# Kernel tuning notes

Hardware: AMD Instinct MI355X
Metric: run time of the kernel (lower is better)

Reference implementation:

```python
import jax, jax.numpy as jnp
import numpy as np

BN_EPS = 1e-5


def setup_inputs() -> dict:
    key = jax.random.key(0)
    ks = jax.random.split(key, 13)
    B, C, H, W = 8, 256, 96, 32
    D = C // 2  # inter_channels
    s = 0.05
    return {
        "x": jax.random.normal(ks[0], (B, C, H, W), jnp.float32),
        "g_w": jax.random.normal(ks[1], (D, C), jnp.float32) * s,
        "g_b": jax.random.normal(ks[2], (D,), jnp.float32) * s,
        "theta_w": jax.random.normal(ks[3], (D, C), jnp.float32) * s,
        "theta_b": jax.random.normal(ks[4], (D,), jnp.float32) * s,
        "phi_w": jax.random.normal(ks[5], (D, C), jnp.float32) * s,
        "phi_b": jax.random.normal(ks[6], (D,), jnp.float32) * s,
        "w_w": jax.random.normal(ks[7], (C, D), jnp.float32) * s,
        "w_b": jax.random.normal(ks[8], (C,), jnp.float32) * s,
        "bn_gamma": jax.random.normal(ks[9], (C,), jnp.float32),
        "bn_beta": jax.random.normal(ks[10], (C,), jnp.float32) * s,
        "bn_mean": jax.random.normal(ks[11], (C,), jnp.float32) * s,
        "bn_var": jax.random.uniform(ks[12], (C,), jnp.float32),
    }


def reference(x, g_w, g_b, theta_w, theta_b, phi_w, phi_b, w_w, w_b,
              bn_gamma, bn_beta, bn_mean, bn_var):
    B, C, H, W = x.shape
    N = H * W
    xf = x.reshape(B, C, N)  # flatten spatial: (B, C, N)

    # 1x1 conv projections == per-pixel linear maps
    g_x = jnp.einsum('dc,bcn->bnd', g_w, xf) + g_b            # (B, N, D)
    theta_x = jnp.einsum('dc,bcn->bnd', theta_w, xf) + theta_b  # (B, N, D)
    phi_x = jnp.einsum('dc,bcn->bdn', phi_w, xf) + phi_b[:, None]  # (B, D, N)

    # unnormalized attention: f = theta phi^T / N, then y = f g
    f_div_C = jnp.einsum('bnd,bdm->bnm', theta_x, phi_x) / N  # (B, N, N)
    y = jnp.einsum('bnm,bmd->bnd', f_div_C, g_x)              # (B, N, D)

    # output 1x1 conv + eval-mode BatchNorm2d
    wy = jnp.einsum('cd,bnd->bcn', w_w, y) + w_b[:, None]     # (B, C, N)
    inv = bn_gamma / jnp.sqrt(bn_var + BN_EPS)
    wy = (wy - bn_mean[:, None]) * inv[:, None] + bn_beta[:, None]

    z = wy.reshape(B, C, H, W) + x  # residual
    return z
```

## Files before the change

kernel.cpp:

```cpp
#include <hip/hip_runtime.h>
#include <hip/hip_bf16.h>
#include <cstddef>

typedef __attribute__((ext_vector_type(8))) short short8;
typedef __attribute__((ext_vector_type(4))) float floatx4;
typedef __hip_bfloat16 bf16;

#define NB 8
#define NC 256
#define ND 128
#define NN 3072
#define BN_EPS 1e-5f
#define MSPLIT 24

static __device__ __forceinline__ short f2s(float v) {
    bf16 h = __float2bfloat16(v);
    return *reinterpret_cast<short*>(&h);
}

__global__ __launch_bounds__(256) void setup_kernel(
    const float* __restrict__ phi_w, const float* __restrict__ g_w,
    const float* __restrict__ theta_w,
    const float* __restrict__ phi_b, const float* __restrict__ g_b,
    const float* __restrict__ theta_b,
    const float* __restrict__ w_b, const float* __restrict__ gamma,
    const float* __restrict__ beta, const float* __restrict__ mean,
    const float* __restrict__ var,
    short* __restrict__ Wall, float* __restrict__ bcat384,
    float* __restrict__ invv, float* __restrict__ bias2,
    float* __restrict__ Mbuf)
{
    int t = threadIdx.x;
    int r = blockIdx.x;
    if (r < 384) {
        const float* src = (r < ND) ? (phi_w + (size_t)r * NC)
                         : (r < NC) ? (g_w + (size_t)(r - ND) * NC)
                                    : (theta_w + (size_t)(r - NC) * NC);
        Wall[(size_t)r * NC + t] = f2s(src[t]);
        if (t == 0)
            bcat384[r] = (r < ND) ? phi_b[r]
                       : (r < NC) ? g_b[r - ND] : theta_b[r - NC];
        if (r == 0) {
            float iv = gamma[t] * rsqrtf(var[t] + BN_EPS);
            invv[t] = iv;
            bias2[t] = iv * (w_b[t] - mean[t]) + beta[t];
        }
    } else {
        floatx4 z = {0.f, 0.f, 0.f, 0.f};
        *(floatx4*)(Mbuf + ((size_t)(r - 384) * 256 + t) * 4) = z;
    }
}

__global__ __launch_bounds__(768)
void proj_kernel(const float* __restrict__ x, const short* __restrict__ Wall,
                 const float* __restrict__ bcat384,
                 short* __restrict__ projbuf, short* __restrict__ thND)
{
    __shared__ short Xs[128][72];
    int b = blockIdx.y;
    int n0 = blockIdx.x * 128;
    int t = threadIdx.x;
    int lane = t & 63;
    int wave = t >> 6;
    int wm = wave >> 1;
    int wn = wave & 1;
    int lm = lane & 15;
    int lk = (lane >> 4) * 8;
    int sn = t & 127;
    int scg = t >> 7;

    const float* xb = x + (size_t)b * NC * NN;

    floatx4 zero = {0.f, 0.f, 0.f, 0.f};
    floatx4 acc[4][4];
#pragma unroll
    for (int i = 0; i < 4; ++i)
#pragma unroll
        for (int j = 0; j < 4; ++j) acc[i][j] = zero;

    for (int kt = 0; kt < NC; kt += 64) {
        __syncthreads();
        if (scg < 4) {
            const float* src = xb + (size_t)(kt + scg * 16) * NN + n0 + sn;
            float v[16];
#pragma unroll
            for (int j = 0; j < 16; ++j) v[j] = src[(size_t)j * NN];
            short8 s0, s1;
#pragma unroll
            for (int j = 0; j < 8; ++j) { s0[j] = f2s(v[j]); s1[j] = f2s(v[8 + j]); }
            *(short8*)&Xs[sn][scg * 16]     = s0;
            *(short8*)&Xs[sn][scg * 16 + 8] = s1;
        }
        __syncthreads();
#pragma unroll
        for (int kk = 0; kk < 64; kk += 32) {
            short8 af[4], bfr[4];
#pragma unroll
            for (int i = 0; i < 4; ++i)
                af[i] = *(const short8*)(Wall +
                        (size_t)(wm * 64 + i * 16 + lm) * NC + kt + kk + lk);
#pragma unroll
            for (int j = 0; j < 4; ++j)
                bfr[j] = *(const short8*)&Xs[wn * 64 + j * 16 + lm][kk + lk];
#pragma unroll
            for (int i = 0; i < 4; ++i)
#pragma unroll
                for (int j = 0; j < 4; ++j)
                    acc[i][j] = __builtin_amdgcn_mfma_f32_16x16x32_bf16(
                        af[i], bfr[j], acc[i][j], 0, 0, 0);
        }
    }

    int row0 = wm * 64 + (lane >> 4) * 4;
    int col0 = n0 + wn * 64 + lm;

    if (wm < 4) {
        short* Cb = projbuf + (size_t)b * NC * NN;
#pragma unroll
        for (int i = 0; i < 4; ++i) {
#pragma unroll
            for (int r = 0; r < 4; ++r) {
                int row = row0 + i * 16 + r;
                float bv = bcat384[row];
#pragma unroll
                for (int j = 0; j < 4; ++j)
                    Cb[(size_t)row * NN + col0 + j * 16] =
                        f2s(acc[i][j][r] + bv);
            }
        }
    } else {
        short* Tb = thND + (size_t)b * NN * ND;
#pragma unroll
        for (int i = 0; i < 4; ++i) {
#pragma unroll
            for (int r = 0; r < 4; ++r) {
                int d = row0 - 256 + i * 16 + r;
                float bv = bcat384[256 + d];
#pragma unroll
                for (int j = 0; j < 4; ++j)
                    Tb[(size_t)(col0 + j * 16) * ND + d] =
                        f2s(acc[i][j][r] + bv);
            }
        }
    }
}

__global__ __launch_bounds__(256)
void bt_gemm(const short* __restrict__ Ag0, const short* __restrict__ Bg0,
             void* __restrict__ Cout, const float* __restrict__ bias,
             const float* __restrict__ resid,
             int M, int N, int K,
             long sA, long sB, long sC, long sR,
             int mode)
{
    __shared__ short As[128][72];
    __shared__ short Bs[128][72];
    int b = blockIdx.z;
    const short* Ag = Ag0 + (size_t)b * sA;
    const short* Bg = Bg0 + (size_t)b * sB;
    int tile_m = blockIdx.y * 128;
    int tile_n = blockIdx.x * 128;
    int t = threadIdx.x;
    int lane = t & 63;
    int wave = t >> 6;
    int wr = wave >> 1, wc = wave & 1;
    int lm = lane & 15;
    int lk = (lane >> 4) * 8;
    int ch = (t & 7) * 8;
    int r0 = t >> 3;

    floatx4 zero = {0.f, 0.f, 0.f, 0.f};
    floatx4 acc[4][4];
#pragma unroll
    for (int i = 0; i < 4; ++i)
#pragma unroll
        for (int j = 0; j < 4; ++j) acc[i][j] = zero;

    for (int kt = 0; kt < K; kt += 64) {
        __syncthreads();
#pragma unroll
        for (int p = 0; p < 4; ++p) {
            int r = r0 + p * 32;
            *(short8*)&As[r][ch] = *(const short8*)(Ag + (size_t)(tile_m + r) * K + kt + ch);
            *(short8*)&Bs[r][ch] = *(const short8*)(Bg + (size_t)(tile_n + r) * K + kt + ch);
        }
        __syncthreads();
#pragma unroll
        for (int kk = 0; kk < 64; kk += 32) {
            short8 af[4], bfr[4];
#pragma unroll
            for (int i = 0; i < 4; ++i)
                af[i] = *(const short8*)&As[wr * 64 + i * 16 + lm][kk + lk];
#pragma unroll
            for (int j = 0; j < 4; ++j)
                bfr[j] = *(const short8*)&Bs[wc * 64 + j * 16 + lm][kk + lk];
#pragma unroll
            for (int i = 0; i < 4; ++i)
#pragma unroll
                for (int j = 0; j < 4; ++j)
                    acc[i][j] = __builtin_amdgcn_mfma_f32_16x16x32_bf16(
                        af[i], bfr[j], acc[i][j], 0, 0, 0);
        }
    }

    int row0 = tile_m + wr * 64 + (lane >> 4) * 4;
    int col0 = tile_n + wc * 64 + lm;

    if (mode == 3) {
        float* Cf = (float*)Cout + (size_t)b * sC;
        const float* Rg = resid + (size_t)b * sR;
#pragma unroll
        for (int i = 0; i < 4; ++i) {
#pragma unroll
            for (int r = 0; r < 4; ++r) {
                int row = row0 + i * 16 + r;
                float bv = bias[row];
#pragma unroll
                for (int j = 0; j < 4; ++j) {
                    size_t idx = (size_t)row * N + col0 + j * 16;
                    Cf[idx] = acc[i][j][r] + bv + Rg[idx];
                }
            }
        }
    }
}

__global__ __launch_bounds__(256)
void mbuf_split(const short* __restrict__ projbuf, float* __restrict__ Mbuf,
                float scale)
{
    __shared__ short As[128][72];
    __shared__ short Bs[128][72];
    int b = blockIdx.z;
    const short* Ag = projbuf + (size_t)b * NC * NN;
    const short* Bg = Ag + (size_t)ND * NN;
    int kt0 = blockIdx.x * (NN / MSPLIT);
    int t = threadIdx.x;
    int lane = t & 63;
    int wave = t >> 6;
    int wr = wave >> 1, wc = wave & 1;
    int lm = lane & 15;
    int lk = (lane >> 4) * 8;
    int ch = (t & 7) * 8;
    int r0 = t >> 3;

    floatx4 zero = {0.f, 0.f, 0.f, 0.f};
    floatx4 acc[4][4];
#pragma unroll
    for (int i = 0; i < 4; ++i)
#pragma unroll
        for (int j = 0; j < 4; ++j) acc[i][j] = zero;

    for (int kt = kt0; kt < kt0 + NN / MSPLIT; kt += 64) {
        __syncthreads();
#pragma unroll
        for (int p = 0; p < 4; ++p) {
            int r = r0 + p * 32;
            *(short8*)&As[r][ch] = *(const short8*)(Ag + (size_t)r * NN + kt + ch);
            *(short8*)&Bs[r][ch] = *(const short8*)(Bg + (size_t)r * NN + kt + ch);
        }
        __syncthreads();
#pragma unroll
        for (int kk = 0; kk < 64; kk += 32) {
            short8 af[4], bfr[4];
#pragma unroll
            for (int i = 0; i < 4; ++i)
                af[i] = *(const short8*)&As[wr * 64 + i * 16 + lm][kk + lk];
#pragma unroll
            for (int j = 0; j < 4; ++j)
                bfr[j] = *(const short8*)&Bs[wc * 64 + j * 16 + lm][kk + lk];
#pragma unroll
            for (int i = 0; i < 4; ++i)
#pragma unroll
                for (int j = 0; j < 4; ++j)
                    acc[i][j] = __builtin_amdgcn_mfma_f32_16x16x32_bf16(
                        af[i], bfr[j], acc[i][j], 0, 0, 0);
        }
    }

    float* Mf = Mbuf + (size_t)b * ND * ND;
    int row0 = wr * 64 + (lane >> 4) * 4;
    int col0 = wc * 64 + lm;
#pragma unroll
    for (int i = 0; i < 4; ++i)
#pragma unroll
        for (int j = 0; j < 4; ++j)
#pragma unroll
            for (int r = 0; r < 4; ++r)
                atomicAdd(&Mf[(size_t)(row0 + i * 16 + r) * ND + col0 + j * 16],
                          acc[i][j][r] * scale);
}

__global__ __launch_bounds__(256)
void p2_kernel(const float* __restrict__ w_w, const float* __restrict__ Mbuf,
               const float* __restrict__ invv, short* __restrict__ P2)
{
    int b = blockIdx.y;
    int t = threadIdx.x;
    int c = blockIdx.x * 2 + (t >> 7);
    int e = t & 127;
    const float* wrow = w_w + (size_t)c * ND;
    const float* Mr = Mbuf + (size_t)b * ND * ND + (size_t)e * ND;
    float s = 0.f;
#pragma unroll 4
    for (int d = 0; d < ND; ++d) s += wrow[d] * Mr[d];
    P2[(size_t)b * NC * ND + (size_t)c * ND + e] = f2s(s * invv[c]);
}

extern "C" void kernel_launch(void* const* d_in, const int* in_sizes, int n_in,
                              void* d_out, int out_size, void* d_ws, size_t ws_size,
                              hipStream_t stream)
{
    const float* x       = (const float*)d_in[0];
    const float* g_w     = (const float*)d_in[1];
    const float* g_b     = (const float*)d_in[2];
    const float* theta_w = (const float*)d_in[3];
    const float* theta_b = (const float*)d_in[4];
    const float* phi_w   = (const float*)d_in[5];
    const float* phi_b   = (const float*)d_in[6];
    const float* w_w     = (const float*)d_in[7];
    const float* w_b     = (const float*)d_in[8];
    const float* gamma   = (const float*)d_in[9];
    const float* beta    = (const float*)d_in[10];
    const float* mean    = (const float*)d_in[11];
    const float* var     = (const float*)d_in[12];
    (void)in_sizes; (void)n_in; (void)out_size; (void)ws_size;

    char* w = (char*)d_ws;
    short* Wall   = (short*)w; w += (size_t)384 * NC * 2;
    float* bcat384= (float*)w; w += (size_t)384 * 4;
    float* invv   = (float*)w; w += (size_t)NC * 4;
    float* bias2  = (float*)w; w += (size_t)NC * 4;
    w = (char*)(((size_t)w + 255) & ~(size_t)255);
    short* projbuf= (short*)w; w += (size_t)NB * NC * NN * 2;
    short* thND   = (short*)w; w += (size_t)NB * NN * ND * 2;
    float* Mbuf   = (float*)w; w += (size_t)NB * ND * ND * 4;
    short* P2     = (short*)w; w += (size_t)NB * NC * ND * 2;

    setup_kernel<<<dim3(384 + 1024), dim3(256), 0, stream>>>(
        phi_w, g_w, theta_w, phi_b, g_b, theta_b, w_b, gamma, beta, mean, var,
        Wall, bcat384, invv, bias2, Mbuf);

    proj_kernel<<<dim3(NN / 128, NB), dim3(768), 0, stream>>>(
        x, Wall, bcat384, projbuf, thND);

    mbuf_split<<<dim3(MSPLIT, 1, NB), 256, 0, stream>>>(
        projbuf, Mbuf, 1.f / (float)NN);

    p2_kernel<<<dim3(NC / 2, NB), 256, 0, stream>>>(w_w, Mbuf, invv, P2);

    bt_gemm<<<dim3(NN / 128, NC / 128, NB), 256, 0, stream>>>(
        P2, thND, d_out, bias2, x,
        NC, NN, ND, (long)NC * ND, (long)NN * ND, (long)NC * NN, (long)NC * NN,
        3);
}
```

Measured before the change: 163.8 us.

## Fold output conv weights into g projection and drop p2 kernel

```diff
diff --git a/kernel.cpp b/kernel.cpp
--- a/kernel.cpp
+++ b/kernel.cpp
@@ -11,7 +11,7 @@
 #define ND 128
 #define NN 3072
 #define BN_EPS 1e-5f
-#define MSPLIT 24
+#define PSPLIT 16
 
 static __device__ __forceinline__ short f2s(float v) {
     bf16 h = __float2bfloat16(v);
@@ -23,51 +23,63 @@
     const float* __restrict__ theta_w,
     const float* __restrict__ phi_b, const float* __restrict__ g_b,
     const float* __restrict__ theta_b,
-    const float* __restrict__ w_b, const float* __restrict__ gamma,
-    const float* __restrict__ beta, const float* __restrict__ mean,
-    const float* __restrict__ var,
-    short* __restrict__ Wall, float* __restrict__ bcat384,
-    float* __restrict__ invv, float* __restrict__ bias2,
-    float* __restrict__ Mbuf)
-{
+    const float* __restrict__ w_w, const float* __restrict__ w_b,
+    const float* __restrict__ gamma, const float* __restrict__ beta,
+    const float* __restrict__ mean, const float* __restrict__ var,
+    short* __restrict__ Wall2, float* __restrict__ bcat512,
+    float* __restrict__ bias2, float* __restrict__ P2acc)
+{
+    __shared__ float red[128];
     int t = threadIdx.x;
     int r = blockIdx.x;
-    if (r < 384) {
-        const float* src = (r < ND) ? (phi_w + (size_t)r * NC)
-                         : (r < NC) ? (g_w + (size_t)(r - ND) * NC)
-                                    : (theta_w + (size_t)(r - NC) * NC);
-        Wall[(size_t)r * NC + t] = f2s(src[t]);
-        if (t == 0)
-            bcat384[r] = (r < ND) ? phi_b[r]
-                       : (r < NC) ? g_b[r - ND] : theta_b[r - NC];
-        if (r == 0) {
-            float iv = gamma[t] * rsqrtf(var[t] + BN_EPS);
-            invv[t] = iv;
-            bias2[t] = iv * (w_b[t] - mean[t]) + beta[t];
-        }
+    if (r < 128) {
+        Wall2[(size_t)r * NC + t] = f2s(phi_w[(size_t)r * NC + t]);
+        if (t == 0) bcat512[r] = phi_b[r];
+    } else if (r < 384) {
+        int c = r - 128;
+        float iv = gamma[c] * rsqrtf(var[c] + BN_EPS);
+        const float* wr = w_w + (size_t)c * ND;
+        float s = 0.f;
+        for (int d = 0; d < ND; ++d)
+            s += wr[d] * g_w[(size_t)d * NC + t];
+        Wall2[(size_t)r * NC + t] = f2s(iv * s);
+        if (t < 128) red[t] = wr[t] * g_b[t];
+        __syncthreads();
+        for (int off = 64; off > 0; off >>= 1) {
+            if (t < off) red[t] += red[t + off];
+            __syncthreads();
+        }
+        if (t == 0) bcat512[r] = iv * red[0];
+    } else if (r < 512) {
+        int d = r - 384;
+        Wall2[(size_t)r * NC + t] = f2s(theta_w[(size_t)d * NC + t]);
+        if (t == 0) bcat512[r] = theta_b[d];
+    } else if (r < 576) {
+        floatx4 z = {0.f, 0.f, 0.f, 0.f};
+        float* p = P2acc + ((size_t)(r - 512) * 256 + t) * 16;
+#pragma unroll
+        for (int j = 0; j < 4; ++j) *(floatx4*)(p + 4 * j) = z;
     } else {
-        floatx4 z = {0.f, 0.f, 0.f, 0.f};
-        *(floatx4*)(Mbuf + ((size_t)(r - 384) * 256 + t) * 4) = z;
-    }
-}
-
-__global__ __launch_bounds__(768)
-void proj_kernel(const float* __restrict__ x, const short* __restrict__ Wall,
-                 const float* __restrict__ bcat384,
+        float iv = gamma[t] * rsqrtf(var[t] + BN_EPS);
+        bias2[t] = iv * (w_b[t] - mean[t]) + beta[t];
+    }
+}
+
+__global__ __launch_bounds__(512)
+void proj_kernel(const float* __restrict__ x, const short* __restrict__ Wall2,
+                 const float* __restrict__ bcat512,
                  short* __restrict__ projbuf, short* __restrict__ thND)
 {
-    __shared__ short Xs[128][72];
+    __shared__ short Xs[64][72];
     int b = blockIdx.y;
-    int n0 = blockIdx.x * 128;
+    int n0 = blockIdx.x * 64;
     int t = threadIdx.x;
     int lane = t & 63;
     int wave = t >> 6;
-    int wm = wave >> 1;
-    int wn = wave & 1;
     int lm = lane & 15;
     int lk = (lane >> 4) * 8;
-    int sn = t & 127;
-    int scg = t >> 7;
+    int sn = t & 63;
+    int scg = t >> 6;
 
     const float* xb = x + (size_t)b * NC * NN;
 
@@ -78,18 +90,15 @@
 #pragma unroll
         for (int j = 0; j < 4; ++j) acc[i][j] = zero;
 
+#pragma unroll
     for (int kt = 0; kt < NC; kt += 64) {
         __syncthreads();
-        if (scg < 4) {
-            const float* src = xb + (size_t)(kt + scg * 16) * NN + n0 + sn;
-            float v[16];
-#pragma unroll
-            for (int j = 0; j < 16; ++j) v[j] = src[(size_t)j * NN];
-            short8 s0, s1;
-#pragma unroll
-            for (int j = 0; j < 8; ++j) { s0[j] = f2s(v[j]); s1[j] = f2s(v[8 + j]); }
-            *(short8*)&Xs[sn][scg * 16]     = s0;
-            *(short8*)&Xs[sn][scg * 16 + 8] = s1;
+        {
+            const float* src = xb + (size_t)(kt + scg * 8) * NN + n0 + sn;
+            short8 s;
+#pragma unroll
+            for (int j = 0; j < 8; ++j) s[j] = f2s(src[(size_t)j * NN]);
+            *(short8*)&Xs[sn][scg * 8] = s;
         }
         __syncthreads();
 #pragma unroll
@@ -97,11 +106,11 @@
             short8 af[4], bfr[4];
 #pragma unroll
             for (int i = 0; i < 4; ++i)
-                af[i] = *(const short8*)(Wall +
-                        (size_t)(wm * 64 + i * 16 + lm) * NC + kt + kk + lk);
+                af[i] = *(const short8*)(Wall2 +
+                        (size_t)(wave * 64 + i * 16 + lm) * NC + kt + kk + lk);
 #pragma unroll
             for (int j = 0; j < 4; ++j)
-                bfr[j] = *(const short8*)&Xs[wn * 64 + j * 16 + lm][kk + lk];
+                bfr[j] = *(const short8*)&Xs[j * 16 + lm][kk + lk];
 #pragma unroll
             for (int i = 0; i < 4; ++i)
 #pragma unroll
@@ -111,17 +120,17 @@
         }
     }
 
-    int row0 = wm * 64 + (lane >> 4) * 4;
-    int col0 = n0 + wn * 64 + lm;
-
-    if (wm < 4) {
-        short* Cb = projbuf + (size_t)b * NC * NN;
+    int row0 = wave * 64 + (lane >> 4) * 4;
+    int col0 = n0 + lm;
+
+    if (wave < 6) {
+        short* Cb = projbuf + (size_t)b * 384 * NN;
 #pragma unroll
         for (int i = 0; i < 4; ++i) {
 #pragma unroll
             for (int r = 0; r < 4; ++r) {
                 int row = row0 + i * 16 + r;
-                float bv = bcat384[row];
+                float bv = bcat512[row];
 #pragma unroll
                 for (int j = 0; j < 4; ++j)
                     Cb[(size_t)row * NN + col0 + j * 16] =
@@ -134,8 +143,9 @@
         for (int i = 0; i < 4; ++i) {
 #pragma unroll
             for (int r = 0; r < 4; ++r) {
-                int d = row0 - 256 + i * 16 + r;
-                float bv = bcat384[256 + d];
+                int row = row0 + i * 16 + r;
+                int d = row - 384;
+                float bv = bcat512[row];
 #pragma unroll
                 for (int j = 0; j < 4; ++j)
                     Tb[(size_t)(col0 + j * 16) * ND + d] =
@@ -146,18 +156,83 @@
 }
 
 __global__ __launch_bounds__(256)
-void bt_gemm(const short* __restrict__ Ag0, const short* __restrict__ Bg0,
-             void* __restrict__ Cout, const float* __restrict__ bias,
-             const float* __restrict__ resid,
-             int M, int N, int K,
-             long sA, long sB, long sC, long sR,
-             int mode)
+void p2split(const short* __restrict__ projbuf, float* __restrict__ P2acc,
+             float scale)
 {
     __shared__ short As[128][72];
     __shared__ short Bs[128][72];
     int b = blockIdx.z;
-    const short* Ag = Ag0 + (size_t)b * sA;
-    const short* Bg = Bg0 + (size_t)b * sB;
+    const short* base = projbuf + (size_t)b * 384 * NN;
+    const short* Ag = base + (size_t)128 * NN;
+    const short* Bg = base;
+    int tile_m = blockIdx.y * 128;
+    int kt0 = blockIdx.x * (NN / PSPLIT);
+    int t = threadIdx.x;
+    int lane = t & 63;
+    int wave = t >> 6;
+    int wr = wave >> 1, wc = wave & 1;
+    int lm = lane & 15;
+    int lk = (lane >> 4) * 8;
+    int ch = (t & 7) * 8;
+    int r0 = t >> 3;
+
+    floatx4 zero = {0.f, 0.f, 0.f, 0.f};
+    floatx4 acc[4][4];
+#pragma unroll
+    for (int i = 0; i < 4; ++i)
+#pragma unroll
+        for (int j = 0; j < 4; ++j) acc[i][j] = zero;
+
+    for (int kt = kt0; kt < kt0 + NN / PSPLIT; kt += 64) {
+        __syncthreads();
+#pragma unroll
+        for (int p = 0; p < 4; ++p) {
+            int r = r0 + p * 32;
+            *(short8*)&As[r][ch] = *(const short8*)(Ag + (size_t)(tile_m + r) * NN + kt + ch);
+            *(short8*)&Bs[r][ch] = *(const short8*)(Bg + (size_t)r * NN + kt + ch);
+        }
+        __syncthreads();
+#pragma unroll
+        for (int kk = 0; kk < 64; kk += 32) {
+            short8 af[4], bfr[4];
+#pragma unroll
+            for (int i = 0; i < 4; ++i)
+                af[i] = *(const short8*)&As[wr * 64 + i * 16 + lm][kk + lk];
+#pragma unroll
+            for (int j = 0; j < 4; ++j)
+                bfr[j] = *(const short8*)&Bs[wc * 64 + j * 16 + lm][kk + lk];
+#pragma unroll
+            for (int i = 0; i < 4; ++i)
+#pragma unroll
+                for (int j = 0; j < 4; ++j)
+                    acc[i][j] = __builtin_amdgcn_mfma_f32_16x16x32_bf16(
+                        af[i], bfr[j], acc[i][j], 0, 0, 0);
+        }
+    }
+
+    float* Pf = P2acc + (size_t)b * NC * ND;
+    int row0 = tile_m + wr * 64 + (lane >> 4) * 4;
+    int col0 = wc * 64 + lm;
+#pragma unroll
+    for (int i = 0; i < 4; ++i)
+#pragma unroll
+        for (int j = 0; j < 4; ++j)
+#pragma unroll
+            for (int r = 0; r < 4; ++r)
+                atomicAdd(&Pf[(size_t)(row0 + i * 16 + r) * ND + col0 + j * 16],
+                          acc[i][j][r] * scale);
+}
+
+__global__ __launch_bounds__(256)
+void final_gemm(const float* __restrict__ P2acc, const short* __restrict__ thND,
+                float* __restrict__ out, const float* __restrict__ bias2,
+                const float* __restrict__ x)
+{
+    __shared__ short As[128][72];
+    __shared__ short Bs[128][72];
+    int b = blockIdx.z;
+    const float* Ag = P2acc + (size_t)b * NC * ND;
+    const short* Bg = thND + (size_t)b * NN * ND;
     int tile_m = blockIdx.y * 128;
     int tile_n = blockIdx.x * 128;
     int t = threadIdx.x;
@@ -176,13 +251,20 @@
 #pragma unroll
         for (int j = 0; j < 4; ++j) acc[i][j] = zero;
 
-    for (int kt = 0; kt < K; kt += 64) {
+#pragma unroll
+    for (int kt = 0; kt < ND; kt += 64) {
         __syncthreads();
 #pragma unroll
         for (int p = 0; p < 4; ++p) {
             int r = r0 + p * 32;
-            *(short8*)&As[r][ch] = *(const short8*)(Ag + (size_t)(tile_m + r) * K + kt + ch);
-            *(short8*)&Bs[r][ch] = *(const short8*)(Bg + (size_t)(tile_n + r) * K + kt + ch);
+            const float* ap = Ag + (size_t)(tile_m + r) * ND + kt + ch;
+            floatx4 v0 = *(const floatx4*)ap;
+            floatx4 v1 = *(const floatx4*)(ap + 4);
+            short8 s;
+#pragma unroll
+            for (int j = 0; j < 4; ++j) { s[j] = f2s(v0[j]); s[4 + j] = f2s(v1[j]); }
+            *(short8*)&As[r][ch] = s;
+            *(short8*)&Bs[r][ch] = *(const short8*)(Bg + (size_t)(tile_n + r) * ND + kt + ch);
         }
         __syncthreads();
 #pragma unroll
@@ -205,106 +287,21 @@
 
     int row0 = tile_m + wr * 64 + (lane >> 4) * 4;
     int col0 = tile_n + wc * 64 + lm;
-
-    if (mode == 3) {
-        float* Cf = (float*)Cout + (size_t)b * sC;
-        const float* Rg = resid + (size_t)b * sR;
-#pragma unroll
-        for (int i = 0; i < 4; ++i) {
-#pragma unroll
-            for (int r = 0; r < 4; ++r) {
-                int row = row0 + i * 16 + r;
-                float bv = bias[row];
-#pragma unroll
-                for (int j = 0; j < 4; ++j) {
-                    size_t idx = (size_t)row * N + col0 + j * 16;
-                    Cf[idx] = acc[i][j][r] + bv + Rg[idx];
-                }
+    float* Cf = out + (size_t)b * NC * NN;
+    const float* Rg = x + (size_t)b * NC * NN;
+#pragma unroll
+    for (int i = 0; i < 4; ++i) {
+#pragma unroll
+        for (int r = 0; r < 4; ++r) {
+            int row = row0 + i * 16 + r;
+            float bv = bias2[row];
+#pragma unroll
+            for (int j = 0; j < 4; ++j) {
+                size_t idx = (size_t)row * NN + col0 + j * 16;
+                Cf[idx] = acc[i][j][r] + bv + Rg[idx];
             }
         }
     }
-}
-
-__global__ __launch_bounds__(256)
-void mbuf_split(const short* __restrict__ projbuf, float* __restrict__ Mbuf,
-                float scale)
-{
-    __shared__ short As[128][72];
-    __shared__ short Bs[128][72];
-    int b = blockIdx.z;
-    const short* Ag = projbuf + (size_t)b * NC * NN;
-    const short* Bg = Ag + (size_t)ND * NN;
-    int kt0 = blockIdx.x * (NN / MSPLIT);
-    int t = threadIdx.x;
-    int lane = t & 63;
-    int wave = t >> 6;
-    int wr = wave >> 1, wc = wave & 1;
-    int lm = lane & 15;
-    int lk = (lane >> 4) * 8;
-    int ch = (t & 7) * 8;
-    int r0 = t >> 3;
-
-    floatx4 zero = {0.f, 0.f, 0.f, 0.f};
-    floatx4 acc[4][4];
-#pragma unroll
-    for (int i = 0; i < 4; ++i)
-#pragma unroll
-        for (int j = 0; j < 4; ++j) acc[i][j] = zero;
-
-    for (int kt = kt0; kt < kt0 + NN / MSPLIT; kt += 64) {
-        __syncthreads();
-#pragma unroll
-        for (int p = 0; p < 4; ++p) {
-            int r = r0 + p * 32;
-            *(short8*)&As[r][ch] = *(const short8*)(Ag + (size_t)r * NN + kt + ch);
-            *(short8*)&Bs[r][ch] = *(const short8*)(Bg + (size_t)r * NN + kt + ch);
-        }
-        __syncthreads();
-#pragma unroll
-        for (int kk = 0; kk < 64; kk += 32) {
-            short8 af[4], bfr[4];
-#pragma unroll
-            for (int i = 0; i < 4; ++i)
-                af[i] = *(const short8*)&As[wr * 64 + i * 16 + lm][kk + lk];
-#pragma unroll
-            for (int j = 0; j < 4; ++j)
-                bfr[j] = *(const short8*)&Bs[wc * 64 + j * 16 + lm][kk + lk];
-#pragma unroll
-            for (int i = 0; i < 4; ++i)
-#pragma unroll
-                for (int j = 0; j < 4; ++j)
-                    acc[i][j] = __builtin_amdgcn_mfma_f32_16x16x32_bf16(
-                        af[i], bfr[j], acc[i][j], 0, 0, 0);
-        }
-    }
-
-    float* Mf = Mbuf + (size_t)b * ND * ND;
-    int row0 = wr * 64 + (lane >> 4) * 4;
-    int col0 = wc * 64 + lm;
-#pragma unroll
-    for (int i = 0; i < 4; ++i)
-#pragma unroll
-        for (int j = 0; j < 4; ++j)
-#pragma unroll
-            for (int r = 0; r < 4; ++r)
-                atomicAdd(&Mf[(size_t)(row0 + i * 16 + r) * ND + col0 + j * 16],
-                          acc[i][j][r] * scale);
-}
-
-__global__ __launch_bounds__(256)
-void p2_kernel(const float* __restrict__ w_w, const float* __restrict__ Mbuf,
-               const float* __restrict__ invv, short* __restrict__ P2)
-{
-    int b = blockIdx.y;
-    int t = threadIdx.x;
-    int c = blockIdx.x * 2 + (t >> 7);
-    int e = t & 127;
-    const float* wrow = w_w + (size_t)c * ND;
-    const float* Mr = Mbuf + (size_t)b * ND * ND + (size_t)e * ND;
-    float s = 0.f;
-#pragma unroll 4
-    for (int d = 0; d < ND; ++d) s += wrow[d] * Mr[d];
-    P2[(size_t)b * NC * ND + (size_t)c * ND + e] = f2s(s * invv[c]);
 }
 
 extern "C" void kernel_launch(void* const* d_in, const int* in_sizes, int n_in,
@@ -327,30 +324,24 @@
     (void)in_sizes; (void)n_in; (void)out_size; (void)ws_size;
 
     char* w = (char*)d_ws;
-    short* Wall   = (short*)w; w += (size_t)384 * NC * 2;
-    float* bcat384= (float*)w; w += (size_t)384 * 4;
-    float* invv   = (float*)w; w += (size_t)NC * 4;
+    short* Wall2  = (short*)w; w += (size_t)512 * NC * 2;
+    float* bcat512= (float*)w; w += (size_t)512 * 4;
     float* bias2  = (float*)w; w += (size_t)NC * 4;
     w = (char*)(((size_t)w + 255) & ~(size_t)255);
-    short* projbuf= (short*)w; w += (size_t)NB * NC * NN * 2;
+    short* projbuf= (short*)w; w += (size_t)NB * 384 * NN * 2;
     short* thND   = (short*)w; w += (size_t)NB * NN * ND * 2;
-    float* Mbuf   = (float*)w; w += (size_t)NB * ND * ND * 4;
-    short* P2     = (short*)w; w += (size_t)NB * NC * ND * 2;
-
-    setup_kernel<<<dim3(384 + 1024), dim3(256), 0, stream>>>(
-        phi_w, g_w, theta_w, phi_b, g_b, theta_b, w_b, gamma, beta, mean, var,
-        Wall, bcat384, invv, bias2, Mbuf);
-
-    proj_kernel<<<dim3(NN / 128, NB), dim3(768), 0, stream>>>(
-        x, Wall, bcat384, projbuf, thND);
-
-    mbuf_split<<<dim3(MSPLIT, 1, NB), 256, 0, stream>>>(
-        projbuf, Mbuf, 1.f / (float)NN);
-
-    p2_kernel<<<dim3(NC / 2, NB), 256, 0, stream>>>(w_w, Mbuf, invv, P2);
-
-    bt_gemm<<<dim3(NN / 128, NC / 128, NB), 256, 0, stream>>>(
-        P2, thND, d_out, bias2, x,
-        NC, NN, ND, (long)NC * ND, (long)NN * ND, (long)NC * NN, (long)NC * NN,
-        3);
-}
+    float* P2acc  = (float*)w; w += (size_t)NB * NC * ND * 4;
+
+    setup_kernel<<<dim3(577), dim3(256), 0, stream>>>(
+        phi_w, g_w, theta_w, phi_b, g_b, theta_b, w_w, w_b,
+        gamma, beta, mean, var, Wall2, bcat512, bias2, P2acc);
+
+    proj_kernel<<<dim3(NN / 64, NB), dim3(512), 0, stream>>>(
+        x, Wall2, bcat512, projbuf, thND);
+
+    p2split<<<dim3(PSPLIT, 2, NB), 256, 0, stream>>>(
+        projbuf, P2acc, 1.f / (float)NN);
+
+    final_gemm<<<dim3(NN / 128, NC / 128, NB), 256, 0, stream>>>(
+        P2acc, thND, (float*)d_out, bias2, x);
+}
```

New measurement: 173.8 us. +6.1%, slower.
